# Kernel optimization log

Measured on AMD Instinct MI355X. Metric: run time of the kernel, lower is better.

## Reference

```python
import jax, jax.numpy as jnp
import numpy as np

N_NODES = 50000
N_EDGES = 800000
IN_DIM = 128
HEADS = 8
F_OUT = 16


def setup_inputs() -> dict:
    key = jax.random.key(0)
    ks = jax.random.split(key, 7)
    x = jax.random.normal(ks[0], (N_NODES, IN_DIM), dtype=jnp.float32)
    edge_index = jax.random.randint(ks[1], (2, N_EDGES), 0, N_NODES, dtype=jnp.int32)
    # xavier-normal-ish scale
    W_proj = jax.random.normal(ks[2], (HEADS * F_OUT, IN_DIM), dtype=jnp.float32) * (2.0 / (IN_DIM + HEADS * F_OUT)) ** 0.5
    a_src = jax.random.normal(ks[3], (HEADS, F_OUT), dtype=jnp.float32) * 0.1
    a_tgt = jax.random.normal(ks[4], (HEADS, F_OUT), dtype=jnp.float32) * 0.1
    W_skip = jax.random.normal(ks[5], (HEADS * F_OUT, IN_DIM), dtype=jnp.float32) * (2.0 / (IN_DIM + HEADS * F_OUT)) ** 0.5
    bias = jnp.zeros((HEADS * F_OUT,), dtype=jnp.float32)
    return {"x": x, "edge_index": edge_index, "W_proj": W_proj, "a_src": a_src,
            "a_tgt": a_tgt, "W_skip": W_skip, "bias": bias}


def reference(x, edge_index, W_proj, a_src, a_tgt, W_skip, bias):
    N = x.shape[0]
    src, tgt = edge_index[0], edge_index[1]
    # project: [N, H, F]
    proj = (x @ W_proj.T).reshape(N, HEADS, F_OUT)
    # per-node partial scores: [N, H]
    s_src = jnp.einsum('nhf,hf->nh', proj, a_src)
    s_tgt = jnp.einsum('nhf,hf->nh', proj, a_tgt)
    # per-edge scores, LeakyReLU(0.2): [E, H]
    e = jax.nn.leaky_relu(s_src[src] + s_tgt[tgt], negative_slope=0.2)
    # segment softmax over incoming edges of each target node
    e_max = jax.ops.segment_max(e, tgt, num_segments=N)
    e_exp = jnp.exp(e - e_max[tgt])
    denom = jax.ops.segment_sum(e_exp, tgt, num_segments=N)
    alpha = e_exp / (denom[tgt] + 1e-16)  # [E, H]
    # weighted scatter-add of projected source features: [N, H, F]
    msgs = proj[src] * alpha[:, :, None]
    out = jax.ops.segment_sum(msgs, tgt, num_segments=N)
    # skip connection (in_dim != out_dim path -> skip_proj), concat heads, bias, ELU
    out = out + (x @ W_skip.T).reshape(N, HEADS, F_OUT)
    out = out.reshape(N, HEADS * F_OUT) + bias
    return jax.nn.elu(out)
```

## Files before the change

kernel.cpp:

```cpp
#include <hip/hip_runtime.h>
#include <hip/hip_bf16.h>
#include <math.h>

#define PADN 50048
#define CAP 64

typedef __attribute__((ext_vector_type(8))) short short8;
typedef __attribute__((ext_vector_type(4))) float f32x4;

__device__ __forceinline__ unsigned short f2b(float f) {
  __hip_bfloat16 h = __float2bfloat16(f);
  return *(unsigned short*)&h;
}

__global__ __launch_bounds__(256) void k_init(const float* __restrict__ Wp,
                                              const float* __restrict__ Ws,
                                              const float* __restrict__ a_src,
                                              const float* __restrict__ a_tgt,
                                              unsigned short* __restrict__ Bpk,
                                              int* __restrict__ counts,
                                              int N, int zeroB) {
  const int b = blockIdx.x;
  if (b < zeroB) {
    int i = b * 256 + threadIdx.x;
    if (i < N) counts[i] = 0;
    return;
  }
  int idx = (b - zeroB) * 256 + threadIdx.x;
  int tile = idx >> 8;
  int ks = (idx >> 6) & 3;
  int lane = idx & 63;
  int kbase = ks * 32 + (lane >> 4) * 8;
  unsigned short o[8];
  if (tile < 16) {
    int col = tile * 16 + (lane & 15);
    const float* src = (col < 128) ? (Wp + (size_t)col * 128 + kbase)
                                   : (Ws + (size_t)(col - 128) * 128 + kbase);
#pragma unroll
    for (int j = 0; j < 8; ++j) o[j] = f2b(src[j]);
  } else {
    int col = lane & 15;
    int h = col & 7;
    const float* av = (col < 8) ? (a_src + h * 16) : (a_tgt + h * 16);
#pragma unroll
    for (int j = 0; j < 8; ++j) {
      int k = kbase + j;
      float s = 0.f;
#pragma unroll
      for (int f = 0; f < 16; ++f) s = fmaf(Wp[(size_t)(h * 16 + f) * 128 + k], av[f], s);
      o[j] = f2b(s);
    }
  }
  *(short8*)(Bpk + (size_t)idx * 8) = *(short8*)o;
}

__global__ __launch_bounds__(256) void k_cg(
    const float* __restrict__ x, const unsigned short* __restrict__ Bpk,
    unsigned short* __restrict__ pb, unsigned short* __restrict__ sb,
    float* __restrict__ ssrc, float* __restrict__ stgt,
    const int* __restrict__ ei, int* __restrict__ counts,
    int* __restrict__ esrc, int N, int E, int cntB) {
  const int b = blockIdx.x;
  if (b < cntB) {
    const int tid = b * 256 + threadIdx.x;
    const int T = cntB * 256;
    const int* srcp = ei;
    const int* tgtp = ei + E;
    int e[8], s[8], t[8], r[8];
#pragma unroll
    for (int p = 0; p < 8; ++p) {
      e[p] = tid + p * T;
      t[p] = (e[p] < E) ? tgtp[e[p]] : 0;
      s[p] = (e[p] < E) ? srcp[e[p]] : 0;
    }
#pragma unroll
    for (int p = 0; p < 8; ++p)
      r[p] = (e[p] < E) ? atomicAdd(&counts[t[p]], 1) : CAP;
#pragma unroll
    for (int p = 0; p < 8; ++p)
      if (r[p] < CAP && e[p] < E) esrc[(t[p] << 6) + r[p]] = s[p];
    return;
  }

  const int wave = threadIdx.x >> 6, lane = threadIdx.x & 63;
  const int m = lane & 15, q = lane >> 4;
  const int r0 = (b - cntB) * 128 + wave * 32;

  short8 a[2][4];
#pragma unroll
  for (int g = 0; g < 2; ++g) {
    const int row_a = r0 + g * 16 + m;
#pragma unroll
    for (int ks = 0; ks < 4; ++ks) {
      float4 v0 = make_float4(0.f, 0.f, 0.f, 0.f), v1 = v0;
      if (row_a < N) {
        const float4* xp = (const float4*)(x + (size_t)row_a * 128 + ks * 32 + q * 8);
        v0 = xp[0];
        v1 = xp[1];
      }
      unsigned short o[8];
      o[0] = f2b(v0.x); o[1] = f2b(v0.y); o[2] = f2b(v0.z); o[3] = f2b(v0.w);
      o[4] = f2b(v1.x); o[5] = f2b(v1.y); o[6] = f2b(v1.z); o[7] = f2b(v1.w);
      a[g][ks] = *(short8*)o;
    }
  }

#define LOADB(dst, t)                                                        \
  {                                                                          \
    const unsigned short* bp_ = Bpk + (size_t)((t) * 256 + lane) * 8;        \
    dst[0] = *(const short8*)(bp_ + 0 * 512);                                \
    dst[1] = *(const short8*)(bp_ + 1 * 512);                                \
    dst[2] = *(const short8*)(bp_ + 2 * 512);                                \
    dst[3] = *(const short8*)(bp_ + 3 * 512);                                \
  }

  short8 bb[2][4];
  LOADB(bb[0], 0)
#pragma unroll
  for (int ct = 0; ct < 17; ++ct) {
    if (ct < 16) LOADB(bb[(ct + 1) & 1], ct + 1)
    f32x4 acc0 = {0.f, 0.f, 0.f, 0.f};
    f32x4 acc1 = {0.f, 0.f, 0.f, 0.f};
#pragma unroll
    for (int ks = 0; ks < 4; ++ks) {
      acc0 = __builtin_amdgcn_mfma_f32_16x16x32_bf16(a[0][ks], bb[ct & 1][ks], acc0, 0, 0, 0);
      acc1 = __builtin_amdgcn_mfma_f32_16x16x32_bf16(a[1][ks], bb[ct & 1][ks], acc1, 0, 0, 0);
    }
    if (ct < 16) {
      unsigned short* dst = (ct < 8) ? pb : sb;
      const int cc = (ct & 7) * 16 + m;
#pragma unroll
      for (int r = 0; r < 4; ++r) {
        int row0 = r0 + q * 4 + r;
        if (row0 < N) dst[(size_t)row0 * 128 + cc] = f2b(acc0[r]);
        int row1 = r0 + 16 + q * 4 + r;
        if (row1 < N) dst[(size_t)row1 * 128 + cc] = f2b(acc1[r]);
      }
    } else {
      float* sd = (m < 8) ? ssrc : stgt;
      const int h = m & 7;
#pragma unroll
      for (int r = 0; r < 4; ++r) {
        int row0 = r0 + q * 4 + r;
        if (row0 < N) sd[row0 * 8 + h] = acc0[r];
        int row1 = r0 + 16 + q * 4 + r;
        if (row1 < N) sd[row1 * 8 + h] = acc1[r];
      }
    }
  }
#undef LOADB
}

__global__ __launch_bounds__(256) void k_agg(const unsigned short* __restrict__ pb,
                                             const unsigned short* __restrict__ sb,
                                             const float* __restrict__ ssrc,
                                             const float* __restrict__ stgt,
                                             const float* __restrict__ bias,
                                             const int* __restrict__ counts,
                                             const int* __restrict__ esrc,
                                             float* __restrict__ out, int N) {
  int wid = (int)((blockIdx.x * (size_t)blockDim.x + threadIdx.x) >> 6);
  int lane = threadIdx.x & 63;
  if (wid >= N) return;
  const int n = wid;
  const int c = lane * 2;
  const int h = lane >> 3;

  const float st = stgt[n * 8 + h];
  const int cnt = min(counts[n], CAP);

  float ds0 = 0.f, ds1 = 0.f, ds2 = 0.f, ds3 = 0.f;
  float x00 = 0.f, x01 = 0.f, x10 = 0.f, x11 = 0.f;
  float x20 = 0.f, x21 = 0.f, x30 = 0.f, x31 = 0.f;

#define FILLQ(p, jj)                                              \
  {                                                               \
    int s_ = __builtin_amdgcn_readlane(srcv, (jj));               \
    pv##p = *(const unsigned int*)(pb + (size_t)s_ * 128 + c);    \
    sc##p = ssrc[s_ * 8 + h];                                     \
  }
#define EDGEQ(p, dsx, a0x, a1x)                                   \
  {                                                               \
    float e_ = sc##p + st;                                        \
    e_ = fmaxf(e_, 0.2f * e_);                                    \
    float w_ = __expf(e_);                                        \
    dsx += w_;                                                    \
    a0x = fmaf(w_, __uint_as_float(pv##p << 16), a0x);            \
    a1x = fmaf(w_, __uint_as_float(pv##p & 0xffff0000u), a1x);    \
  }

  if (cnt > 0) {
    const int cm = cnt - 1;
    int srcv = esrc[(n << 6) + min(lane, cm)];
    unsigned int pv0, pv1, pv2, pv3, pv4, pv5, pv6, pv7;
    float sc0, sc1, sc2, sc3, sc4, sc5, sc6, sc7;

    FILLQ(0, 0)
    FILLQ(1, min(1, cm))
    FILLQ(2, min(2, cm))
    FILLQ(3, min(3, cm))
    FILLQ(4, min(4, cm))
    FILLQ(5, min(5, cm))
    FILLQ(6, min(6, cm))
    FILLQ(7, min(7, cm))

    int j = 0;
    for (; j + 8 <= cnt; j += 8) {
      EDGEQ(0, ds0, x00, x01)
      EDGEQ(1, ds1, x10, x11)
      EDGEQ(2, ds2, x20, x21)
      EDGEQ(3, ds3, x30, x31)
      if (j + 8 < cnt) {
        FILLQ(0, min(j + 8, cm))
        FILLQ(1, min(j + 9, cm))
        FILLQ(2, min(j + 10, cm))
        FILLQ(3, min(j + 11, cm))
      }
      EDGEQ(4, ds0, x00, x01)
      EDGEQ(5, ds1, x10, x11)
      EDGEQ(6, ds2, x20, x21)
      EDGEQ(7, ds3, x30, x31)
      if (j + 12 < cnt) {
        FILLQ(4, min(j + 12, cm))
        FILLQ(5, min(j + 13, cm))
        FILLQ(6, min(j + 14, cm))
        FILLQ(7, min(j + 15, cm))
      }
    }
    const int rem = cnt - j;
    if (rem > 0) EDGEQ(0, ds0, x00, x01)
    if (rem > 1) EDGEQ(1, ds1, x10, x11)
    if (rem > 2) EDGEQ(2, ds2, x20, x21)
    if (rem > 3) EDGEQ(3, ds3, x30, x31)
    if (rem > 4) EDGEQ(4, ds0, x00, x01)
    if (rem > 5) EDGEQ(5, ds1, x10, x11)
    if (rem > 6) EDGEQ(6, ds2, x20, x21)
  }
#undef FILLQ
#undef EDGEQ

  const float dsum = (ds0 + ds1) + (ds2 + ds3);
  const float acc0 = (x00 + x10) + (x20 + x30);
  const float acc1 = (x01 + x11) + (x21 + x31);
  const float inv = 1.0f / (dsum + 1e-16f);
  size_t row = (size_t)n * 128;
  unsigned int su = *(const unsigned int*)(sb + row + c);
  float sk0 = __uint_as_float(su << 16);
  float sk1 = __uint_as_float(su & 0xffff0000u);
  float r0 = fmaf(acc0, inv, sk0) + bias[c];
  float r1 = fmaf(acc1, inv, sk1) + bias[c + 1];
  r0 = (r0 > 0.f) ? r0 : (__expf(r0) - 1.0f);
  r1 = (r1 > 0.f) ? r1 : (__expf(r1) - 1.0f);
  *(float2*)(out + row + c) = make_float2(r0, r1);
}

extern "C" void kernel_launch(void* const* d_in, const int* in_sizes, int n_in,
                              void* d_out, int out_size, void* d_ws, size_t ws_size,
                              hipStream_t stream) {
  const float* x = (const float*)d_in[0];
  const int* ei = (const int*)d_in[1];
  const float* Wp = (const float*)d_in[2];
  const float* a_src = (const float*)d_in[3];
  const float* a_tgt = (const float*)d_in[4];
  const float* Ws = (const float*)d_in[5];
  const float* bias = (const float*)d_in[6];
  float* out = (float*)d_out;

  const int N = in_sizes[0] / 128;
  const int E = in_sizes[1] / 2;

  unsigned short* Bpk = (unsigned short*)d_ws;
  unsigned short* pb = Bpk + 34816;
  unsigned short* sb = pb + (size_t)N * 128;
  float* ssrc = (float*)(sb + (size_t)N * 128);
  float* stgt = ssrc + (size_t)N * 8;
  int* counts = (int*)(stgt + (size_t)N * 8);
  int* esrc = counts + N;

  const int zeroB = (N + 255) / 256;
  const int cntB = (E + 8 * 256 - 1) / (8 * 256);
  const int gemmB = PADN / 128;

  k_init<<<zeroB + 17, 256, 0, stream>>>(Wp, Ws, a_src, a_tgt, Bpk, counts, N, zeroB);
  k_cg<<<cntB + gemmB, 256, 0, stream>>>(x, Bpk, pb, sb, ssrc, stgt, ei, counts,
                                         esrc, N, E, cntB);
  k_agg<<<(N + 3) / 4, 256, 0, stream>>>(pb, sb, ssrc, stgt, bias, counts, esrc, out, N);
}
```

Baseline: 184.7 us.

## Partition edge bucketing by XCD target range and use nontemporal loads/stores

The edge-bucketing blocks are reorganised so each block handles an edge slice but only the targets in one of eight node ranges, selected by block index modulo 8. The intent is that atomics and esrc writes for a given node range stay on one XCD's L2, cutting cross-die coherence traffic. The cost is that every edge is read eight times, once by the matching block on each XCD. Loads of x and stores of pb, sb and the score arrays in the GEMM path become nontemporal to reduce cache pollution. The node split is hardcoded as GRP=6250 and SLICE=16384, so it is tied to N=50000.

```diff
diff --git a/kernel.cpp b/kernel.cpp
--- a/kernel.cpp
+++ b/kernel.cpp
@@ -4,9 +4,13 @@
 
 #define PADN 50048
 #define CAP 64
+#define NXCD 8
+#define GRP 6250
+#define SLICE 16384
 
 typedef __attribute__((ext_vector_type(8))) short short8;
 typedef __attribute__((ext_vector_type(4))) float f32x4;
+typedef __attribute__((ext_vector_type(4))) int int4v;
 
 __device__ __forceinline__ unsigned short f2b(float f) {
   __hip_bfloat16 h = __float2bfloat16(f);
@@ -62,23 +66,29 @@
     int* __restrict__ esrc, int N, int E, int cntB) {
   const int b = blockIdx.x;
   if (b < cntB) {
-    const int tid = b * 256 + threadIdx.x;
-    const int T = cntB * 256;
+    const int g = b & (NXCD - 1);
+    const int sl = b >> 3;
+    const int lo = g * GRP;
+    const int hi = lo + GRP;
+    const int base = sl * SLICE;
     const int* srcp = ei;
     const int* tgtp = ei + E;
-    int e[8], s[8], t[8], r[8];
-#pragma unroll
-    for (int p = 0; p < 8; ++p) {
-      e[p] = tid + p * T;
-      t[p] = (e[p] < E) ? tgtp[e[p]] : 0;
-      s[p] = (e[p] < E) ? srcp[e[p]] : 0;
-    }
-#pragma unroll
-    for (int p = 0; p < 8; ++p)
-      r[p] = (e[p] < E) ? atomicAdd(&counts[t[p]], 1) : CAP;
-#pragma unroll
-    for (int p = 0; p < 8; ++p)
-      if (r[p] < CAP && e[p] < E) esrc[(t[p] << 6) + r[p]] = s[p];
+#pragma unroll
+    for (int it = 0; it < 16; ++it) {
+      int e0 = base + (it * 256 + threadIdx.x) * 4;
+      if (e0 < E) {
+        int4v t4 = __builtin_nontemporal_load((const int4v*)(tgtp + e0));
+        int4v s4 = __builtin_nontemporal_load((const int4v*)(srcp + e0));
+#pragma unroll
+        for (int k = 0; k < 4; ++k) {
+          int t = t4[k];
+          if (t >= lo && t < hi) {
+            int r = atomicAdd(&counts[t], 1);
+            if (r < CAP) esrc[(t << 6) + r] = s4[k];
+          }
+        }
+      }
+    }
     return;
   }
 
@@ -92,15 +102,15 @@
     const int row_a = r0 + g * 16 + m;
 #pragma unroll
     for (int ks = 0; ks < 4; ++ks) {
-      float4 v0 = make_float4(0.f, 0.f, 0.f, 0.f), v1 = v0;
+      f32x4 v0 = {0.f, 0.f, 0.f, 0.f}, v1 = v0;
       if (row_a < N) {
-        const float4* xp = (const float4*)(x + (size_t)row_a * 128 + ks * 32 + q * 8);
-        v0 = xp[0];
-        v1 = xp[1];
+        const f32x4* xp = (const f32x4*)(x + (size_t)row_a * 128 + ks * 32 + q * 8);
+        v0 = __builtin_nontemporal_load(xp);
+        v1 = __builtin_nontemporal_load(xp + 1);
       }
       unsigned short o[8];
-      o[0] = f2b(v0.x); o[1] = f2b(v0.y); o[2] = f2b(v0.z); o[3] = f2b(v0.w);
-      o[4] = f2b(v1.x); o[5] = f2b(v1.y); o[6] = f2b(v1.z); o[7] = f2b(v1.w);
+      o[0] = f2b(v0[0]); o[1] = f2b(v0[1]); o[2] = f2b(v0[2]); o[3] = f2b(v0[3]);
+      o[4] = f2b(v1[0]); o[5] = f2b(v1[1]); o[6] = f2b(v1[2]); o[7] = f2b(v1[3]);
       a[g][ks] = *(short8*)o;
     }
   }
@@ -132,9 +142,9 @@
 #pragma unroll
       for (int r = 0; r < 4; ++r) {
         int row0 = r0 + q * 4 + r;
-        if (row0 < N) dst[(size_t)row0 * 128 + cc] = f2b(acc0[r]);
+        if (row0 < N) __builtin_nontemporal_store(f2b(acc0[r]), &dst[(size_t)row0 * 128 + cc]);
         int row1 = r0 + 16 + q * 4 + r;
-        if (row1 < N) dst[(size_t)row1 * 128 + cc] = f2b(acc1[r]);
+        if (row1 < N) __builtin_nontemporal_store(f2b(acc1[r]), &dst[(size_t)row1 * 128 + cc]);
       }
     } else {
       float* sd = (m < 8) ? ssrc : stgt;
@@ -142,9 +152,9 @@
 #pragma unroll
       for (int r = 0; r < 4; ++r) {
         int row0 = r0 + q * 4 + r;
-        if (row0 < N) sd[row0 * 8 + h] = acc0[r];
+        if (row0 < N) __builtin_nontemporal_store(acc0[r], &sd[row0 * 8 + h]);
         int row1 = r0 + 16 + q * 4 + r;
-        if (row1 < N) sd[row1 * 8 + h] = acc1[r];
+        if (row1 < N) __builtin_nontemporal_store(acc1[r], &sd[row1 * 8 + h]);
       }
     }
   }
@@ -278,7 +288,8 @@
   int* esrc = counts + N;
 
   const int zeroB = (N + 255) / 256;
-  const int cntB = (E + 8 * 256 - 1) / (8 * 256);
+  const int nsl = (E + SLICE - 1) / SLICE;
+  const int cntB = nsl * NXCD;
   const int gemmB = PADN / 128;
 
   k_init<<<zeroB + 17, 256, 0, stream>>>(Wp, Ws, a_src, a_tgt, Bpk, counts, N, zeroB);
```

Measured after the change: 208.7 us. +13.0%, slower.

## Shard per-node edge counters four ways and split binning from GEMM kernel

Applied to the files above, without the earlier changes.

Replaces the single atomic counter per target node with four sharded counters, each owning a 16-slot sub-bucket of the 64-slot edge list, so contended atomics spread across addresses. A thread whose shard is full falls back to probing the other shards. The aggregation kernel compacts the four sub-buckets with a ballot into shared memory before use. The fused bin+GEMM launch is also split into two separate kernels, which adds a launch and removes overlap between the two phases.

```diff
diff --git a/kernel.cpp b/kernel.cpp
--- a/kernel.cpp
+++ b/kernel.cpp
@@ -4,6 +4,8 @@
 
 #define PADN 50048
 #define CAP 64
+#define NSH 4
+#define SHCAP 16
 
 typedef __attribute__((ext_vector_type(8))) short short8;
 typedef __attribute__((ext_vector_type(4))) float f32x4;
@@ -18,12 +20,12 @@
                                               const float* __restrict__ a_src,
                                               const float* __restrict__ a_tgt,
                                               unsigned short* __restrict__ Bpk,
-                                              int* __restrict__ counts,
-                                              int N, int zeroB) {
+                                              int* __restrict__ counts4,
+                                              int N4, int zeroB) {
   const int b = blockIdx.x;
   if (b < zeroB) {
     int i = b * 256 + threadIdx.x;
-    if (i < N) counts[i] = 0;
+    if (i < N4) counts4[i] = 0;
     return;
   }
   int idx = (b - zeroB) * 256 + threadIdx.x;
@@ -54,37 +56,47 @@
   *(short8*)(Bpk + (size_t)idx * 8) = *(short8*)o;
 }
 
-__global__ __launch_bounds__(256) void k_cg(
+__global__ __launch_bounds__(256) void k_bin(const int* __restrict__ ei,
+                                             int* __restrict__ counts4,
+                                             int* __restrict__ esrc, int E, int T) {
+  const int tid = blockIdx.x * 256 + threadIdx.x;
+  const int s0 = tid & 3;
+  const int* srcp = ei;
+  const int* tgtp = ei + E;
+  int e[8], s[8], t[8], r[8];
+#pragma unroll
+  for (int p = 0; p < 8; ++p) {
+    e[p] = tid + p * T;
+    t[p] = (e[p] < E) ? tgtp[e[p]] : -1;
+    s[p] = (e[p] < E) ? srcp[e[p]] : 0;
+  }
+#pragma unroll
+  for (int p = 0; p < 8; ++p)
+    r[p] = (t[p] >= 0) ? atomicAdd(&counts4[t[p] * 4 + s0], 1) : 0;
+#pragma unroll
+  for (int p = 0; p < 8; ++p) {
+    if (t[p] >= 0) {
+      if (r[p] < SHCAP) {
+        esrc[(t[p] << 6) + s0 * SHCAP + r[p]] = s[p];
+      } else {
+#pragma unroll 1
+        for (int k = 1; k < NSH; ++k) {
+          int ss = (s0 + k) & (NSH - 1);
+          int rr = atomicAdd(&counts4[t[p] * 4 + ss], 1);
+          if (rr < SHCAP) { esrc[(t[p] << 6) + ss * SHCAP + rr] = s[p]; break; }
+        }
+      }
+    }
+  }
+}
+
+__global__ __launch_bounds__(256) void k_gemm(
     const float* __restrict__ x, const unsigned short* __restrict__ Bpk,
     unsigned short* __restrict__ pb, unsigned short* __restrict__ sb,
-    float* __restrict__ ssrc, float* __restrict__ stgt,
-    const int* __restrict__ ei, int* __restrict__ counts,
-    int* __restrict__ esrc, int N, int E, int cntB) {
-  const int b = blockIdx.x;
-  if (b < cntB) {
-    const int tid = b * 256 + threadIdx.x;
-    const int T = cntB * 256;
-    const int* srcp = ei;
-    const int* tgtp = ei + E;
-    int e[8], s[8], t[8], r[8];
-#pragma unroll
-    for (int p = 0; p < 8; ++p) {
-      e[p] = tid + p * T;
-      t[p] = (e[p] < E) ? tgtp[e[p]] : 0;
-      s[p] = (e[p] < E) ? srcp[e[p]] : 0;
-    }
-#pragma unroll
-    for (int p = 0; p < 8; ++p)
-      r[p] = (e[p] < E) ? atomicAdd(&counts[t[p]], 1) : CAP;
-#pragma unroll
-    for (int p = 0; p < 8; ++p)
-      if (r[p] < CAP && e[p] < E) esrc[(t[p] << 6) + r[p]] = s[p];
-    return;
-  }
-
+    float* __restrict__ ssrc, float* __restrict__ stgt, int N) {
   const int wave = threadIdx.x >> 6, lane = threadIdx.x & 63;
   const int m = lane & 15, q = lane >> 4;
-  const int r0 = (b - cntB) * 128 + wave * 32;
+  const int r0 = blockIdx.x * 128 + wave * 32;
 
   short8 a[2][4];
 #pragma unroll
@@ -156,18 +168,30 @@
                                              const float* __restrict__ ssrc,
                                              const float* __restrict__ stgt,
                                              const float* __restrict__ bias,
-                                             const int* __restrict__ counts,
+                                             const int* __restrict__ counts4,
                                              const int* __restrict__ esrc,
                                              float* __restrict__ out, int N) {
+  __shared__ int comp[4][64];
   int wid = (int)((blockIdx.x * (size_t)blockDim.x + threadIdx.x) >> 6);
   int lane = threadIdx.x & 63;
   if (wid >= N) return;
   const int n = wid;
+  const int wv = threadIdx.x >> 6;
   const int c = lane * 2;
   const int h = lane >> 3;
 
   const float st = stgt[n * 8 + h];
-  const int cnt = min(counts[n], CAP);
+
+  int c4 = counts4[n * 4 + (lane >> 4)];
+  bool valid = (lane & 15) < min(c4, SHCAP);
+  int sv = esrc[(n << 6) + lane];
+  unsigned long long mk = __ballot(valid);
+  const int cnt = __popcll(mk);
+  if (valid) {
+    int pos = __popcll(mk & ((1ull << lane) - 1ull));
+    comp[wv][pos] = sv;
+  }
+  __asm__ volatile("s_waitcnt lgkmcnt(0)" ::: "memory");
 
   float ds0 = 0.f, ds1 = 0.f, ds2 = 0.f, ds3 = 0.f;
   float x00 = 0.f, x01 = 0.f, x10 = 0.f, x11 = 0.f;
@@ -191,7 +215,7 @@
 
   if (cnt > 0) {
     const int cm = cnt - 1;
-    int srcv = esrc[(n << 6) + min(lane, cm)];
+    int srcv = comp[wv][lane];
     unsigned int pv0, pv1, pv2, pv3, pv4, pv5, pv6, pv7;
     float sc0, sc1, sc2, sc3, sc4, sc5, sc6, sc7;
 
@@ -274,15 +298,17 @@
   unsigned short* sb = pb + (size_t)N * 128;
   float* ssrc = (float*)(sb + (size_t)N * 128);
   float* stgt = ssrc + (size_t)N * 8;
-  int* counts = (int*)(stgt + (size_t)N * 8);
-  int* esrc = counts + N;
-
-  const int zeroB = (N + 255) / 256;
-  const int cntB = (E + 8 * 256 - 1) / (8 * 256);
+  int* counts4 = (int*)(stgt + (size_t)N * 8);
+  int* esrc = counts4 + (size_t)N * 4;
+
+  const int N4 = N * 4;
+  const int zeroB = (N4 + 255) / 256;
+  const int binB = (E + 8 * 256 - 1) / (8 * 256);
   const int gemmB = PADN / 128;
-
-  k_init<<<zeroB + 17, 256, 0, stream>>>(Wp, Ws, a_src, a_tgt, Bpk, counts, N, zeroB);
-  k_cg<<<cntB + gemmB, 256, 0, stream>>>(x, Bpk, pb, sb, ssrc, stgt, ei, counts,
-                                         esrc, N, E, cntB);
-  k_agg<<<(N + 3) / 4, 256, 0, stream>>>(pb, sb, ssrc, stgt, bias, counts, esrc, out, N);
-}
+  const int T = binB * 256;
+
+  k_init<<<zeroB + 17, 256, 0, stream>>>(Wp, Ws, a_src, a_tgt, Bpk, counts4, N4, zeroB);
+  k_bin<<<binB, 256, 0, stream>>>(ei, counts4, esrc, E, T);
+  k_gemm<<<gemmB, 256, 0, stream>>>(x, Bpk, pb, sb, ssrc, stgt, N);
+  k_agg<<<(N + 3) / 4, 256, 0, stream>>>(pb, sb, ssrc, stgt, bias, counts4, esrc, out, N);
+}
```

Measured after the change: 191.4 us. 1.04x slower.

## Replace global atomic edge bucketing with two-level binned partition into shared memory

Applied to the files above, without the earlier changes.

Edge-to-target bucketing no longer uses per-edge global atomics on a 50K-entry counter array. Each block now partitions 8192 edges into 98 coarse bins using a shared-memory histogram and prefix scan, then writes them to per-bin segments. A new kernel builds each 512-node slice's 64-slot CSR buckets in LDS and writes them out with coalesced stores. Source indices are packed as 16-bit values, which halves the esrc footprint read by aggregation. The cost is an extra kernel launch and a dependence on N < 65536 and fixed segment capacities, so a heavily skewed bin would silently drop edges.

```diff
diff --git a/kernel.cpp b/kernel.cpp
--- a/kernel.cpp
+++ b/kernel.cpp
@@ -4,6 +4,11 @@
 
 #define PADN 50048
 #define CAP 64
+#define NBIN 98
+#define BINSZ 512
+#define SEGCAP 9216
+#define EPB 8192
+#define INVALID 0xFFFFFFFFu
 
 typedef __attribute__((ext_vector_type(8))) short short8;
 typedef __attribute__((ext_vector_type(4))) float f32x4;
@@ -18,15 +23,13 @@
                                               const float* __restrict__ a_src,
                                               const float* __restrict__ a_tgt,
                                               unsigned short* __restrict__ Bpk,
-                                              int* __restrict__ counts,
-                                              int N, int zeroB) {
+                                              int* __restrict__ cursor) {
   const int b = blockIdx.x;
-  if (b < zeroB) {
-    int i = b * 256 + threadIdx.x;
-    if (i < N) counts[i] = 0;
+  if (b == 17) {
+    if (threadIdx.x < NBIN) cursor[threadIdx.x] = threadIdx.x * SEGCAP;
     return;
   }
-  int idx = (b - zeroB) * 256 + threadIdx.x;
+  int idx = b * 256 + threadIdx.x;
   int tile = idx >> 8;
   int ks = (idx >> 6) & 3;
   int lane = idx & 63;
@@ -54,37 +57,76 @@
   *(short8*)(Bpk + (size_t)idx * 8) = *(short8*)o;
 }
 
-__global__ __launch_bounds__(256) void k_cg(
+__global__ __launch_bounds__(256) void k_pg(
     const float* __restrict__ x, const unsigned short* __restrict__ Bpk,
     unsigned short* __restrict__ pb, unsigned short* __restrict__ sb,
     float* __restrict__ ssrc, float* __restrict__ stgt,
-    const int* __restrict__ ei, int* __restrict__ counts,
-    int* __restrict__ esrc, int N, int E, int cntB) {
+    const int* __restrict__ ei, int* __restrict__ cursor,
+    unsigned int* __restrict__ binned, int N, int E, int partB) {
+  __shared__ unsigned int ord[EPB];
+  __shared__ int hist[128], scn[128], base_[128], pos_[128], mybase[128];
   const int b = blockIdx.x;
-  if (b < cntB) {
-    const int tid = b * 256 + threadIdx.x;
-    const int T = cntB * 256;
+  if (b < partB) {
+    const int tid = threadIdx.x;
+    const int e0 = b * EPB;
+    const int ne = min(EPB, E - e0);
     const int* srcp = ei;
     const int* tgtp = ei + E;
-    int e[8], s[8], t[8], r[8];
-#pragma unroll
-    for (int p = 0; p < 8; ++p) {
-      e[p] = tid + p * T;
-      t[p] = (e[p] < E) ? tgtp[e[p]] : 0;
-      s[p] = (e[p] < E) ? srcp[e[p]] : 0;
-    }
-#pragma unroll
-    for (int p = 0; p < 8; ++p)
-      r[p] = (e[p] < E) ? atomicAdd(&counts[t[p]], 1) : CAP;
-#pragma unroll
-    for (int p = 0; p < 8; ++p)
-      if (r[p] < CAP && e[p] < E) esrc[(t[p] << 6) + r[p]] = s[p];
+    if (tid < 128) hist[tid] = 0;
+    __syncthreads();
+    unsigned int pk[32];
+#pragma unroll
+    for (int j = 0; j < 32; ++j) {
+      int e = e0 + j * 256 + tid;
+      if (e < E) {
+        unsigned int t = (unsigned int)tgtp[e];
+        unsigned int s = (unsigned int)srcp[e];
+        pk[j] = (t << 16) | s;
+        atomicAdd(&hist[t >> 9], 1);
+      } else {
+        pk[j] = INVALID;
+      }
+    }
+    __syncthreads();
+    int c = (tid < 128) ? hist[tid] : 0;
+    if (tid < 128) scn[tid] = c;
+    __syncthreads();
+#pragma unroll
+    for (int off = 1; off < 128; off <<= 1) {
+      int v = 0;
+      if (tid < 128 && tid >= off) v = scn[tid - off];
+      __syncthreads();
+      if (tid < 128) scn[tid] += v;
+      __syncthreads();
+    }
+    if (tid < 128) {
+      int eb = scn[tid] - c;
+      base_[tid] = eb;
+      pos_[tid] = eb;
+      mybase[tid] = (tid < NBIN && c > 0) ? atomicAdd(&cursor[tid], c) : 0;
+    }
+    __syncthreads();
+#pragma unroll
+    for (int j = 0; j < 32; ++j) {
+      if (pk[j] != INVALID) {
+        int bb = pk[j] >> 25;
+        int r = atomicAdd(&pos_[bb], 1);
+        ord[r] = pk[j];
+      }
+    }
+    __syncthreads();
+    for (int i = tid; i < ne; i += 256) {
+      unsigned int p = ord[i];
+      int bb = p >> 25;
+      int gpos = mybase[bb] + (i - base_[bb]);
+      if (gpos < (bb + 1) * SEGCAP) binned[gpos] = p;
+    }
     return;
   }
 
   const int wave = threadIdx.x >> 6, lane = threadIdx.x & 63;
   const int m = lane & 15, q = lane >> 4;
-  const int r0 = (b - cntB) * 128 + wave * 32;
+  const int r0 = (b - partB) * 128 + wave * 32;
 
   short8 a[2][4];
 #pragma unroll
@@ -151,13 +193,42 @@
 #undef LOADB
 }
 
+__global__ __launch_bounds__(256) void k_csr(const unsigned int* __restrict__ binned,
+                                             const int* __restrict__ cursor,
+                                             int* __restrict__ counts,
+                                             unsigned short* __restrict__ esrc,
+                                             int N) {
+  extern __shared__ unsigned short buck[];
+  __shared__ int cnt512[BINSZ];
+  const int g = blockIdx.x, tid = threadIdx.x;
+  const int lo = g * BINSZ;
+  for (int i = tid; i < BINSZ; i += 256) cnt512[i] = 0;
+  __syncthreads();
+  const int cnt = min(cursor[g] - g * SEGCAP, SEGCAP);
+  const unsigned int* seg = binned + (size_t)g * SEGCAP;
+  for (int i = tid; i < cnt; i += 256) {
+    unsigned int p = seg[i];
+    int tl = (p >> 16) & (BINSZ - 1);
+    int r = atomicAdd(&cnt512[tl], 1);
+    if (r < CAP) buck[(tl << 6) + r] = (unsigned short)(p & 0xFFFFu);
+  }
+  __syncthreads();
+  uint4* dst = (uint4*)(esrc + ((size_t)lo << 6));
+  const uint4* s4 = (const uint4*)buck;
+  for (int v = tid; v < (BINSZ * CAP) / 8; v += 256) dst[v] = s4[v];
+  for (int i = tid; i < BINSZ; i += 256) {
+    int n = lo + i;
+    if (n < N) counts[n] = min(cnt512[i], CAP);
+  }
+}
+
 __global__ __launch_bounds__(256) void k_agg(const unsigned short* __restrict__ pb,
                                              const unsigned short* __restrict__ sb,
                                              const float* __restrict__ ssrc,
                                              const float* __restrict__ stgt,
                                              const float* __restrict__ bias,
                                              const int* __restrict__ counts,
-                                             const int* __restrict__ esrc,
+                                             const unsigned short* __restrict__ esrc,
                                              float* __restrict__ out, int N) {
   int wid = (int)((blockIdx.x * (size_t)blockDim.x + threadIdx.x) >> 6);
   int lane = threadIdx.x & 63;
@@ -191,7 +262,7 @@
 
   if (cnt > 0) {
     const int cm = cnt - 1;
-    int srcv = esrc[(n << 6) + min(lane, cm)];
+    int srcv = (int)esrc[(n << 6) + min(lane, cm)];
     unsigned int pv0, pv1, pv2, pv3, pv4, pv5, pv6, pv7;
     float sc0, sc1, sc2, sc3, sc4, sc5, sc6, sc7;
 
@@ -275,14 +346,17 @@
   float* ssrc = (float*)(sb + (size_t)N * 128);
   float* stgt = ssrc + (size_t)N * 8;
   int* counts = (int*)(stgt + (size_t)N * 8);
-  int* esrc = counts + N;
-
-  const int zeroB = (N + 255) / 256;
-  const int cntB = (E + 8 * 256 - 1) / (8 * 256);
+  unsigned short* esrcU = (unsigned short*)(counts + N);
+  unsigned int* binned = (unsigned int*)(esrcU + (size_t)NBIN * BINSZ * CAP);
+  int* cursor = (int*)(binned + (size_t)NBIN * SEGCAP);
+
+  const int partB = (E + EPB - 1) / EPB;
   const int gemmB = PADN / 128;
 
-  k_init<<<zeroB + 17, 256, 0, stream>>>(Wp, Ws, a_src, a_tgt, Bpk, counts, N, zeroB);
-  k_cg<<<cntB + gemmB, 256, 0, stream>>>(x, Bpk, pb, sb, ssrc, stgt, ei, counts,
-                                         esrc, N, E, cntB);
-  k_agg<<<(N + 3) / 4, 256, 0, stream>>>(pb, sb, ssrc, stgt, bias, counts, esrc, out, N);
-}
+  k_init<<<18, 256, 0, stream>>>(Wp, Ws, a_src, a_tgt, Bpk, cursor);
+  k_pg<<<partB + gemmB, 256, 0, stream>>>(x, Bpk, pb, sb, ssrc, stgt, ei, cursor,
+                                          binned, N, E, partB);
+  k_csr<<<NBIN, 256, BINSZ * CAP * sizeof(unsigned short), stream>>>(binned, cursor,
+                                                                     counts, esrcU, N);
+  k_agg<<<(N + 3) / 4, 256, 0, stream>>>(pb, sb, ssrc, stgt, bias, counts, esrcU, out, N);
+}
```

Measured after the change: 166.5 us. -9.9%, faster.
